# Performance work log

Hardware: AMD Instinct MI355X
Metric: run time of the kernel (lower is better)

## Reference

```python
import jax, jax.numpy as jnp
import numpy as np

TOP_K = 2

def setup_inputs() -> dict:
    key = jax.random.key(0)
    ks = jax.random.split(key, 8)
    B, S, H, E, F = 4, 2048, 1024, 8, 2048  # F = hidden * expansion(2)
    scale_in = 0.02
    return {
        "x": jax.random.normal(ks[0], (B, S, H), dtype=jnp.float32),
        "router_w": jax.random.normal(ks[1], (H, E), dtype=jnp.float32) * scale_in,
        "router_b": jnp.zeros((E,), dtype=jnp.float32),
        "w1": jax.random.normal(ks[2], (E, H, F), dtype=jnp.float32) * scale_in,
        "b1": jnp.zeros((E, F), dtype=jnp.float32),
        "w2": jax.random.normal(ks[3], (E, F, H), dtype=jnp.float32) * scale_in,
        "b2": jnp.zeros((E, H), dtype=jnp.float32),
    }

def reference(x, router_w, router_b, w1, b1, w2, b2):
    B, S, H = x.shape
    E = router_b.shape[0]
    T = B * S
    flat = x.reshape(T, H)
    # Router + top-k gating (softmax over the k selected logits, as in torch code)
    logits = flat @ router_w + router_b                       # [T, E]
    topk_scores, topk_idx = jax.lax.top_k(logits, TOP_K)      # [T, k]
    probs = jax.nn.softmax(topk_scores, axis=-1)              # [T, k]
    # Dense gate matrix: gates[t, e] = prob if e selected for token t else 0
    gates = jnp.zeros((T, E), dtype=flat.dtype).at[
        jnp.arange(T)[:, None], topk_idx
    ].add(probs)                                              # [T, E]
    # Expert FFNs computed as batched GEMMs over the expert axis
    h = jax.nn.relu(jnp.einsum('td,edf->etf', flat, w1) + b1[:, None, :])  # [E, T, F]
    eout = jnp.einsum('etf,efd->etd', h, w2) + b2[:, None, :]              # [E, T, H]
    out = jnp.einsum('etd,te->td', eout, gates)                            # [T, H]
    return out.reshape(B, S, H)
```

## Files before the change

### kernel.cpp

```cpp
#include <hip/hip_runtime.h>
#include <hip/hip_bf16.h>

#define T_TOK 8192
#define HDIM 1024
#define FDIM 2048
#define NEXP 8
#define NASSIGN (T_TOK * 2)
#define ROWCAP (NASSIGN + 256)
#define NHB 64
#define MAXT 136
#define MAXT2 72

typedef __bf16 bf16;
typedef __bf16 bf16x4 __attribute__((ext_vector_type(4)));
typedef __bf16 bf16x8 __attribute__((ext_vector_type(8)));
typedef float f32x4 __attribute__((ext_vector_type(4)));

__device__ __forceinline__ void gload_lds16(const void* g, void* l) {
    __builtin_amdgcn_global_load_lds(
        (const __attribute__((address_space(1))) void*)(uintptr_t)g,
        (__attribute__((address_space(3))) void*)(uintptr_t)l,
        16, 0, 0);
}

__global__ __launch_bounds__(256) void transpose_to_bf16(
    const float* __restrict__ in, bf16* __restrict__ out, int R, int C) {
    __shared__ float tile[64][68];
    int e = blockIdx.z;
    const float* inp = in + (size_t)e * R * C;
    bf16* outp = out + (size_t)e * R * C;
    int c0 = blockIdx.x * 64, r0 = blockIdx.y * 64;
    int tid = threadIdx.x;
    int tx = tid & 15, ty = tid >> 4;
#pragma unroll
    for (int i = 0; i < 4; i++) {
        int row = ty + i * 16;
        float4 v = *(const float4*)&inp[(size_t)(r0 + row) * C + c0 + tx * 4];
        *(float4*)&tile[row][tx * 4] = v;
    }
    __syncthreads();
#pragma unroll
    for (int i = 0; i < 2; i++) {
        int idx = tid + i * 256;
        int c = idx >> 3, seg = idx & 7;
        bf16x8 v;
#pragma unroll
        for (int j = 0; j < 8; j++) v[j] = (bf16)tile[seg * 8 + j][c];
        *(bf16x8*)&outp[(size_t)(c0 + c) * R + r0 + seg * 8] = v;
    }
}

__global__ __launch_bounds__(256) void router_kernel(
    const float* __restrict__ x, const float* __restrict__ rw,
    const float* __restrict__ rb, int* __restrict__ expert_pair,
    float2* __restrict__ gate_pair) {
    __shared__ float rwT[NEXP][HDIM];
    __shared__ float rbs[NEXP];
    int tid = threadIdx.x;
    for (int i = tid; i < HDIM * NEXP / 4; i += 256) {
        float4 v = ((const float4*)rw)[i];
        int h = i >> 1, e0 = (i & 1) * 4;
        rwT[e0 + 0][h] = v.x;
        rwT[e0 + 1][h] = v.y;
        rwT[e0 + 2][h] = v.z;
        rwT[e0 + 3][h] = v.w;
    }
    if (tid < NEXP) rbs[tid] = rb[tid];
    __syncthreads();
    int wave = tid >> 6, lane = tid & 63;
    int tbase = blockIdx.x * 32 + wave * 8;

    for (int tk = 0; tk < 8; tk++) {
        int t = tbase + tk;
        const float4* xt = (const float4*)(x + (size_t)t * HDIM);
        float p[NEXP];
#pragma unroll
        for (int e = 0; e < NEXP; e++) p[e] = 0.f;
#pragma unroll
        for (int it = 0; it < 4; it++) {
            float4 v = xt[it * 64 + lane];
            int h = (it * 64 + lane) * 4;
#pragma unroll
            for (int e = 0; e < NEXP; e++) {
                float4 wv = *(const float4*)&rwT[e][h];
                p[e] += v.x * wv.x + v.y * wv.y + v.z * wv.z + v.w * wv.w;
            }
        }
#pragma unroll
        for (int off = 32; off >= 1; off >>= 1) {
#pragma unroll
            for (int e = 0; e < NEXP; e++) p[e] += __shfl_xor(p[e], off, 64);
        }
        if (lane == 0) {
            float lg[NEXP];
#pragma unroll
            for (int e = 0; e < NEXP; e++) lg[e] = p[e] + rbs[e];
            int e0 = 0;
#pragma unroll
            for (int e = 1; e < NEXP; e++)
                if (lg[e] > lg[e0]) e0 = e;
            int e1 = -1;
#pragma unroll
            for (int e = 0; e < NEXP; e++) {
                if (e == e0) continue;
                if (e1 < 0 || lg[e] > lg[e1]) e1 = e;
            }
            float z = expf(lg[e1] - lg[e0]);
            expert_pair[t] = e0 | (e1 << 16);
            gate_pair[t] = make_float2(1.f / (1.f + z), z / (1.f + z));
        }
    }
}

__global__ __launch_bounds__(256) void hist_kernel(
    const int* __restrict__ expert_pair, int* __restrict__ hist) {
    int tid = threadIdx.x;
    int wave = tid >> 6, lane = tid & 63;
    int a = blockIdx.x * 256 + tid;
    int t = a >> 1, j = a & 1;
    int e = (expert_pair[t] >> (16 * j)) & 0xffff;
    __shared__ int wcnt[4][NEXP];
#pragma unroll
    for (int ee = 0; ee < NEXP; ee++) {
        unsigned long long m = __ballot(e == ee);
        if (lane == 0) wcnt[wave][ee] = __popcll(m);
    }
    __syncthreads();
    if (tid < NEXP)
        hist[blockIdx.x * NEXP + tid] =
            wcnt[0][tid] + wcnt[1][tid] + wcnt[2][tid] + wcnt[3][tid];
}

__global__ __launch_bounds__(256) void scan_kernel(
    const int* __restrict__ hist, int* __restrict__ start,
    int* __restrict__ cnt, int* __restrict__ offs,
    int* __restrict__ tile_e2, int* __restrict__ tile_m2,
    int* __restrict__ ntiles2) {
    __shared__ int h[NHB * NEXP];
    __shared__ int tot[NEXP];
    __shared__ int offsh[NEXP];
    int tid = threadIdx.x;
    for (int i = tid; i < NHB * NEXP; i += 256) h[i] = hist[i];
    __syncthreads();
    if (tid < NEXP) {
        int s = 0;
        for (int b = 0; b < NHB; b++) s += h[b * NEXP + tid];
        tot[tid] = s;
        cnt[tid] = s;
    }
    __syncthreads();
    if (tid == 0) {
        int o = 0;
        for (int e = 0; e < NEXP; e++) {
            offsh[e] = o;
            offs[e] = o;
            o += tot[e];
        }
        int idx2 = 0;
        for (int e = 0; e < NEXP; e++) {
            int nt = (tot[e] + 255) >> 8;
            for (int m = 0; m < nt; m++) {
                tile_e2[idx2] = e;
                tile_m2[idx2] = m;
                idx2++;
            }
        }
        ntiles2[0] = idx2;
    }
    __syncthreads();
    if (tid < NEXP) {
        int run = offsh[tid];
        for (int b = 0; b < NHB; b++) {
            start[b * NEXP + tid] = run;
            run += h[b * NEXP + tid];
        }
    }
}

__global__ __launch_bounds__(256) void scatter_kernel(
    const int* __restrict__ expert_pair, const float2* __restrict__ gate_pair,
    const int* __restrict__ start, int* __restrict__ perm,
    float* __restrict__ gatebuf, int* __restrict__ rowbuf) {
    int tid = threadIdx.x;
    int wave = tid >> 6, lane = tid & 63;
    int a = blockIdx.x * 256 + tid;
    int t = a >> 1, j = a & 1;
    int e = (expert_pair[t] >> (16 * j)) & 0xffff;
    float2 gp = gate_pair[t];
    float g = j ? gp.y : gp.x;
    __shared__ int wcnt[4][NEXP];
    int rankw = 0;
    unsigned long long below = (1ull << lane) - 1ull;
#pragma unroll
    for (int ee = 0; ee < NEXP; ee++) {
        unsigned long long m = __ballot(e == ee);
        if (lane == 0) wcnt[wave][ee] = __popcll(m);
        if (ee == e) rankw = __popcll(m & below);
    }
    __syncthreads();
    int cross = 0;
    for (int w = 0; w < wave; w++) cross += wcnt[w][e];
    int pos = start[blockIdx.x * NEXP + e] + cross + rankw;
    perm[pos] = t;
    gatebuf[pos] = g;
    rowbuf[a] = pos;
}

__global__ __launch_bounds__(256) void pack_kernel(
    const float* __restrict__ x, const int* __restrict__ perm,
    bf16* __restrict__ xg) {
    int r0 = blockIdx.x * 16;
    int wave = threadIdx.x >> 6, lane = threadIdx.x & 63;
#pragma unroll
    for (int i = 0; i < 4; i++) {
        int row = r0 + wave * 4 + i;
        int tok = perm[row];
        const float* src = x + (size_t)tok * HDIM;
        bf16* dst = xg + (size_t)row * HDIM;
#pragma unroll
        for (int it = 0; it < 4; it++) {
            int c = (it * 64 + lane) * 4;
            float4 v = *(const float4*)&src[c];
            bf16x4 b = {(bf16)v.x, (bf16)v.y, (bf16)v.z, (bf16)v.w};
            *(bf16x4*)&dst[c] = b;
        }
    }
}

template <bool RELU, bool GATE, int K, int N>
__global__ __launch_bounds__(512, 4) void moe_gemm_p(
    const bf16* __restrict__ A, const bf16* __restrict__ B,
    const float* __restrict__ bias, const float* __restrict__ gates,
    bf16* __restrict__ out, const int* __restrict__ cnt,
    const int* __restrict__ offs, const int* __restrict__ tile_e2,
    const int* __restrict__ tile_m2, const int* __restrict__ ntiles2) {
    constexpr int NT = N / 128;
    constexpr int nk = K / 32;
    int ntl = ntiles2[0];
    int nact = ntl * NT;
    int f = blockIdx.x;
    if (f >= nact) return;
    int q8 = nact >> 3, r8 = nact & 7;
    int xcd = f & 7, rest = f >> 3;
    int wg = (xcd < r8) ? (xcd * (q8 + 1) + rest)
                        : (r8 * (q8 + 1) + (xcd - r8) * q8 + rest);
    int tile = wg / NT, ncol = wg - tile * NT;
    int e = tile_e2[tile];
    int n_cnt = cnt[e];
    int off_e = offs[e];
    int m0 = tile_m2[tile] * 256;
    int n0 = ncol * 128;

    __shared__ bf16 As[3][256][32];
    __shared__ bf16 Bs[3][128][32];

    int tid = threadIdx.x;
    int lane = tid & 63;
    int wave = tid >> 6;
    int wm = wave & 1;
    int wn = wave >> 1;
    int quad = lane >> 4, l16 = lane & 15;
    int rsw = (quad ^ ((l16 >> 1) & 3)) * 8;

    const bf16* Ae = A + (size_t)off_e * K;
    const bf16* Be = B + (size_t)e * (size_t)N * K;

    int r0s = tid >> 2;
    int segs = (tid & 3) ^ ((tid >> 3) & 3);
    const bf16* agA0 = Ae + (size_t)(m0 + r0s) * K + segs * 8;
    const bf16* agA1 = Ae + (size_t)(m0 + 128 + r0s) * K + segs * 8;
    const bf16* bgB0 = Be + (size_t)(n0 + r0s) * K + segs * 8;

    auto STG = [&](int buf, int kt) {
        bf16* Ab = (bf16*)As + (size_t)buf * (256 * 32);
        bf16* Bb = (bf16*)Bs + (size_t)buf * (128 * 32);
        gload_lds16(agA0 + (size_t)kt * 32, Ab + (wave * 64) * 8);
        gload_lds16(agA1 + (size_t)kt * 32, Ab + (512 + wave * 64) * 8);
        gload_lds16(bgB0 + (size_t)kt * 32, Bb + (wave * 64) * 8);
    };

    f32x4 acc[8][2];
#pragma unroll
    for (int i = 0; i < 8; i++)
#pragma unroll
        for (int j = 0; j < 2; j++) acc[i][j] = f32x4{0.f, 0.f, 0.f, 0.f};

    STG(0, 0);
    STG(1, 1);

    int b = 0, bs = 2;
    for (int t = 0; t < nk; t++) {
        if (t + 2 < nk) {
            STG(bs, t + 2);
            asm volatile("s_waitcnt vmcnt(6)" ::: "memory");
        } else if (t + 2 == nk) {
            asm volatile("s_waitcnt vmcnt(3)" ::: "memory");
        } else {
            asm volatile("s_waitcnt vmcnt(0)" ::: "memory");
        }
        asm volatile("s_barrier" ::: "memory");

        const bf16* Ab = (const bf16*)As + (size_t)b * (256 * 32);
        const bf16* Bb = (const bf16*)Bs + (size_t)b * (128 * 32);
        bf16x8 bf0 = *(const bf16x8*)(Bb + (wn * 32 + 0 * 16 + l16) * 32 + rsw);
        bf16x8 bf1 = *(const bf16x8*)(Bb + (wn * 32 + 1 * 16 + l16) * 32 + rsw);
        bf16x8 af[4];
#pragma unroll
        for (int mi = 0; mi < 4; mi++)
            af[mi] = *(const bf16x8*)(Ab + (wm * 128 + mi * 16 + l16) * 32 + rsw);
        asm volatile("s_waitcnt lgkmcnt(0)" ::: "memory");
        __builtin_amdgcn_s_setprio(1);
#pragma unroll
        for (int mi = 0; mi < 4; mi++) {
            acc[mi][0] = __builtin_amdgcn_mfma_f32_16x16x32_bf16(af[mi], bf0, acc[mi][0], 0, 0, 0);
            acc[mi][1] = __builtin_amdgcn_mfma_f32_16x16x32_bf16(af[mi], bf1, acc[mi][1], 0, 0, 0);
        }
        __builtin_amdgcn_s_setprio(0);
#pragma unroll
        for (int mi = 0; mi < 4; mi++)
            af[mi] = *(const bf16x8*)(Ab + (wm * 128 + (4 + mi) * 16 + l16) * 32 + rsw);
        asm volatile("s_waitcnt lgkmcnt(0)" ::: "memory");
        __builtin_amdgcn_s_setprio(1);
#pragma unroll
        for (int mi = 0; mi < 4; mi++) {
            acc[4 + mi][0] = __builtin_amdgcn_mfma_f32_16x16x32_bf16(af[mi], bf0, acc[4 + mi][0], 0, 0, 0);
            acc[4 + mi][1] = __builtin_amdgcn_mfma_f32_16x16x32_bf16(af[mi], bf1, acc[4 + mi][1], 0, 0, 0);
        }
        __builtin_amdgcn_s_setprio(0);
        asm volatile("s_barrier" ::: "memory");

        b = (b == 2) ? 0 : b + 1;
        bs = (bs == 2) ? 0 : bs + 1;
    }

#pragma unroll
    for (int mi = 0; mi < 8; mi++)
#pragma unroll
        for (int nj = 0; nj < 2; nj++)
#pragma unroll
            for (int r = 0; r < 4; r++) {
                int m = m0 + wm * 128 + mi * 16 + quad * 4 + r;
                if (m < n_cnt) {
                    int n = n0 + wn * 32 + nj * 16 + l16;
                    float v = acc[mi][nj][r] + bias[e * N + n];
                    if (RELU) v = v > 0.f ? v : 0.f;
                    if (GATE) v *= gates[off_e + m];
                    out[(size_t)(off_e + m) * N + n] = (bf16)v;
                }
            }
}

__global__ __launch_bounds__(256) void combine_kernel(
    const bf16* __restrict__ eout, const int* __restrict__ rowbuf,
    float* __restrict__ out) {
    int t = blockIdx.x;
    int r0 = rowbuf[2 * t], r1 = rowbuf[2 * t + 1];
    const bf16* p0 = eout + (size_t)r0 * HDIM;
    const bf16* p1 = eout + (size_t)r1 * HDIM;
    float* o = out + (size_t)t * HDIM;
    int n = threadIdx.x * 4;
    bf16x4 a = *(const bf16x4*)&p0[n];
    bf16x4 b = *(const bf16x4*)&p1[n];
    float4 v = {(float)a[0] + (float)b[0], (float)a[1] + (float)b[1],
                (float)a[2] + (float)b[2], (float)a[3] + (float)b[3]};
    *(float4*)&o[n] = v;
}

extern "C" void kernel_launch(void* const* d_in, const int* in_sizes, int n_in,
                              void* d_out, int out_size, void* d_ws, size_t ws_size,
                              hipStream_t stream) {
    const float* x = (const float*)d_in[0];
    const float* rw = (const float*)d_in[1];
    const float* rb = (const float*)d_in[2];
    const float* w1 = (const float*)d_in[3];
    const float* b1 = (const float*)d_in[4];
    const float* w2 = (const float*)d_in[5];
    const float* b2 = (const float*)d_in[6];
    float* out = (float*)d_out;

    char* ws = (char*)d_ws;
    size_t o = 0;
    auto alloc = [&](size_t bytes) {
        char* p = ws + o;
        o += (bytes + 255) & ~(size_t)255;
        return p;
    };
    bf16* w1t = (bf16*)alloc((size_t)NEXP * FDIM * HDIM * 2);
    bf16* w2t = (bf16*)alloc((size_t)NEXP * HDIM * FDIM * 2);
    bf16* hbuf = (bf16*)alloc((size_t)ROWCAP * FDIM * 2);
    bf16* xg = (bf16*)alloc((size_t)ROWCAP * HDIM * 2);
    bf16* eout = xg;
    int* expert_pair = (int*)alloc((size_t)T_TOK * 4);
    float2* gate_pair = (float2*)alloc((size_t)T_TOK * 8);
    int* hist = (int*)alloc((size_t)NHB * NEXP * 4);
    int* start = (int*)alloc((size_t)NHB * NEXP * 4);
    int* perm = (int*)alloc((size_t)NASSIGN * 4);
    float* gatebuf = (float*)alloc((size_t)NASSIGN * 4);
    int* rowbuf = (int*)alloc((size_t)NASSIGN * 4);
    int* cnt = (int*)alloc(256);
    int* offs = (int*)alloc(256);
    int* tile_e2 = (int*)alloc((size_t)MAXT2 * 4);
    int* tile_m2 = (int*)alloc((size_t)MAXT2 * 4);
    int* ntiles2 = (int*)alloc(256);

    transpose_to_bf16<<<dim3(FDIM / 64, HDIM / 64, NEXP), 256, 0, stream>>>(w1, w1t, HDIM, FDIM);
    transpose_to_bf16<<<dim3(HDIM / 64, FDIM / 64, NEXP), 256, 0, stream>>>(w2, w2t, FDIM, HDIM);
    router_kernel<<<T_TOK / 32, 256, 0, stream>>>(x, rw, rb, expert_pair, gate_pair);
    hist_kernel<<<NHB, 256, 0, stream>>>(expert_pair, hist);
    scan_kernel<<<1, 256, 0, stream>>>(hist, start, cnt, offs, tile_e2, tile_m2, ntiles2);
    scatter_kernel<<<NHB, 256, 0, stream>>>(expert_pair, gate_pair, start, perm, gatebuf, rowbuf);
    pack_kernel<<<NASSIGN / 16, 256, 0, stream>>>(x, perm, xg);
    moe_gemm_p<true, false, HDIM, FDIM><<<dim3(MAXT2 * (FDIM / 128)), 512, 0, stream>>>(
        xg, w1t, b1, nullptr, hbuf, cnt, offs, tile_e2, tile_m2, ntiles2);
    moe_gemm_p<false, true, FDIM, HDIM><<<dim3(MAXT2 * (HDIM / 128)), 512, 0, stream>>>(
        hbuf, w2t, b2, gatebuf, eout, cnt, offs, tile_e2, tile_m2, ntiles2);
    combine_kernel<<<T_TOK, 256, 0, stream>>>(eout, rowbuf, out);
}
```

Measured before the change: 458.8 us.

## Use 4-wave GEMM blocks with 128x64 per-wave tiles for more register reuse

```diff
diff --git a/kernel.cpp b/kernel.cpp
--- a/kernel.cpp
+++ b/kernel.cpp
@@ -8,7 +8,6 @@
 #define NASSIGN (T_TOK * 2)
 #define ROWCAP (NASSIGN + 256)
 #define NHB 64
-#define MAXT 136
 #define MAXT2 72
 
 typedef __bf16 bf16;
@@ -228,7 +227,7 @@
 }
 
 template <bool RELU, bool GATE, int K, int N>
-__global__ __launch_bounds__(512, 4) void moe_gemm_p(
+__global__ __launch_bounds__(256, 2) void moe_gemm_p(
     const bf16* __restrict__ A, const bf16* __restrict__ B,
     const float* __restrict__ bias, const float* __restrict__ gates,
     bf16* __restrict__ out, const int* __restrict__ cnt,
@@ -267,23 +266,27 @@
 
     int r0s = tid >> 2;
     int segs = (tid & 3) ^ ((tid >> 3) & 3);
-    const bf16* agA0 = Ae + (size_t)(m0 + r0s) * K + segs * 8;
-    const bf16* agA1 = Ae + (size_t)(m0 + 128 + r0s) * K + segs * 8;
-    const bf16* bgB0 = Be + (size_t)(n0 + r0s) * K + segs * 8;
+    const bf16* agA = Ae + (size_t)(m0 + r0s) * K + segs * 8;
+    const bf16* bgB = Be + (size_t)(n0 + r0s) * K + segs * 8;
 
     auto STG = [&](int buf, int kt) {
         bf16* Ab = (bf16*)As + (size_t)buf * (256 * 32);
         bf16* Bb = (bf16*)Bs + (size_t)buf * (128 * 32);
-        gload_lds16(agA0 + (size_t)kt * 32, Ab + (wave * 64) * 8);
-        gload_lds16(agA1 + (size_t)kt * 32, Ab + (512 + wave * 64) * 8);
-        gload_lds16(bgB0 + (size_t)kt * 32, Bb + (wave * 64) * 8);
+#pragma unroll
+        for (int j = 0; j < 4; j++)
+            gload_lds16(agA + (size_t)(j * 64) * K + (size_t)kt * 32,
+                        Ab + wave * 512 + j * 2048);
+#pragma unroll
+        for (int j = 0; j < 2; j++)
+            gload_lds16(bgB + (size_t)(j * 64) * K + (size_t)kt * 32,
+                        Bb + wave * 512 + j * 2048);
     };
 
-    f32x4 acc[8][2];
+    f32x4 acc[8][4];
 #pragma unroll
     for (int i = 0; i < 8; i++)
 #pragma unroll
-        for (int j = 0; j < 2; j++) acc[i][j] = f32x4{0.f, 0.f, 0.f, 0.f};
+        for (int j = 0; j < 4; j++) acc[i][j] = f32x4{0.f, 0.f, 0.f, 0.f};
 
     STG(0, 0);
     STG(1, 1);
@@ -292,9 +295,9 @@
     for (int t = 0; t < nk; t++) {
         if (t + 2 < nk) {
             STG(bs, t + 2);
+            asm volatile("s_waitcnt vmcnt(12)" ::: "memory");
+        } else if (t + 2 == nk) {
             asm volatile("s_waitcnt vmcnt(6)" ::: "memory");
-        } else if (t + 2 == nk) {
-            asm volatile("s_waitcnt vmcnt(3)" ::: "memory");
         } else {
             asm volatile("s_waitcnt vmcnt(0)" ::: "memory");
         }
@@ -302,30 +305,21 @@
 
         const bf16* Ab = (const bf16*)As + (size_t)b * (256 * 32);
         const bf16* Bb = (const bf16*)Bs + (size_t)b * (128 * 32);
-        bf16x8 bf0 = *(const bf16x8*)(Bb + (wn * 32 + 0 * 16 + l16) * 32 + rsw);
-        bf16x8 bf1 = *(const bf16x8*)(Bb + (wn * 32 + 1 * 16 + l16) * 32 + rsw);
-        bf16x8 af[4];
-#pragma unroll
-        for (int mi = 0; mi < 4; mi++)
+        bf16x8 bfv[4];
+#pragma unroll
+        for (int nj = 0; nj < 4; nj++)
+            bfv[nj] = *(const bf16x8*)(Bb + (wn * 64 + nj * 16 + l16) * 32 + rsw);
+        bf16x8 af[8];
+#pragma unroll
+        for (int mi = 0; mi < 8; mi++)
             af[mi] = *(const bf16x8*)(Ab + (wm * 128 + mi * 16 + l16) * 32 + rsw);
-        asm volatile("s_waitcnt lgkmcnt(0)" ::: "memory");
         __builtin_amdgcn_s_setprio(1);
 #pragma unroll
-        for (int mi = 0; mi < 4; mi++) {
-            acc[mi][0] = __builtin_amdgcn_mfma_f32_16x16x32_bf16(af[mi], bf0, acc[mi][0], 0, 0, 0);
-            acc[mi][1] = __builtin_amdgcn_mfma_f32_16x16x32_bf16(af[mi], bf1, acc[mi][1], 0, 0, 0);
-        }
-        __builtin_amdgcn_s_setprio(0);
-#pragma unroll
-        for (int mi = 0; mi < 4; mi++)
-            af[mi] = *(const bf16x8*)(Ab + (wm * 128 + (4 + mi) * 16 + l16) * 32 + rsw);
-        asm volatile("s_waitcnt lgkmcnt(0)" ::: "memory");
-        __builtin_amdgcn_s_setprio(1);
-#pragma unroll
-        for (int mi = 0; mi < 4; mi++) {
-            acc[4 + mi][0] = __builtin_amdgcn_mfma_f32_16x16x32_bf16(af[mi], bf0, acc[4 + mi][0], 0, 0, 0);
-            acc[4 + mi][1] = __builtin_amdgcn_mfma_f32_16x16x32_bf16(af[mi], bf1, acc[4 + mi][1], 0, 0, 0);
-        }
+        for (int mi = 0; mi < 8; mi++)
+#pragma unroll
+            for (int nj = 0; nj < 4; nj++)
+                acc[mi][nj] = __builtin_amdgcn_mfma_f32_16x16x32_bf16(
+                    af[mi], bfv[nj], acc[mi][nj], 0, 0, 0);
         __builtin_amdgcn_s_setprio(0);
         asm volatile("s_barrier" ::: "memory");
 
@@ -336,12 +330,12 @@
 #pragma unroll
     for (int mi = 0; mi < 8; mi++)
 #pragma unroll
-        for (int nj = 0; nj < 2; nj++)
+        for (int nj = 0; nj < 4; nj++)
 #pragma unroll
             for (int r = 0; r < 4; r++) {
                 int m = m0 + wm * 128 + mi * 16 + quad * 4 + r;
                 if (m < n_cnt) {
-                    int n = n0 + wn * 32 + nj * 16 + l16;
+                    int n = n0 + wn * 64 + nj * 16 + l16;
                     float v = acc[mi][nj][r] + bias[e * N + n];
                     if (RELU) v = v > 0.f ? v : 0.f;
                     if (GATE) v *= gates[off_e + m];
@@ -410,9 +404,9 @@
     scan_kernel<<<1, 256, 0, stream>>>(hist, start, cnt, offs, tile_e2, tile_m2, ntiles2);
     scatter_kernel<<<NHB, 256, 0, stream>>>(expert_pair, gate_pair, start, perm, gatebuf, rowbuf);
     pack_kernel<<<NASSIGN / 16, 256, 0, stream>>>(x, perm, xg);
-    moe_gemm_p<true, false, HDIM, FDIM><<<dim3(MAXT2 * (FDIM / 128)), 512, 0, stream>>>(
+    moe_gemm_p<true, false, HDIM, FDIM><<<dim3(MAXT2 * (FDIM / 128)), 256, 0, stream>>>(
         xg, w1t, b1, nullptr, hbuf, cnt, offs, tile_e2, tile_m2, ntiles2);
-    moe_gemm_p<false, true, FDIM, HDIM><<<dim3(MAXT2 * (HDIM / 128)), 512, 0, stream>>>(
+    moe_gemm_p<false, true, FDIM, HDIM><<<dim3(MAXT2 * (HDIM / 128)), 256, 0, stream>>>(
         hbuf, w2t, b2, gatebuf, eout, cnt, offs, tile_e2, tile_m2, ntiles2);
     combine_kernel<<<T_TOK, 256, 0, stream>>>(eout, rowbuf, out);
 }
```

After: 493.9 us. +7.7%, slower.

## Fuse histogram and bf16 cast into router, gather rows inside first GEMM

Applied to the files above, without the earlier changes.

```diff
diff --git a/kernel.cpp b/kernel.cpp
--- a/kernel.cpp
+++ b/kernel.cpp
@@ -7,8 +7,7 @@
 #define NEXP 8
 #define NASSIGN (T_TOK * 2)
 #define ROWCAP (NASSIGN + 256)
-#define NHB 64
-#define MAXT 136
+#define NHB 256
 #define MAXT2 72
 
 typedef __bf16 bf16;
@@ -53,9 +52,11 @@
 __global__ __launch_bounds__(256) void router_kernel(
     const float* __restrict__ x, const float* __restrict__ rw,
     const float* __restrict__ rb, int* __restrict__ expert_pair,
-    float2* __restrict__ gate_pair) {
+    float2* __restrict__ gate_pair, bf16* __restrict__ xb,
+    int* __restrict__ hist) {
     __shared__ float rwT[NEXP][HDIM];
     __shared__ float rbs[NEXP];
+    __shared__ int sh_pair[32];
     int tid = threadIdx.x;
     for (int i = tid; i < HDIM * NEXP / 4; i += 256) {
         float4 v = ((const float4*)rw)[i];
@@ -79,6 +80,8 @@
 #pragma unroll
         for (int it = 0; it < 4; it++) {
             float4 v = xt[it * 64 + lane];
+            bf16x4 bv = {(bf16)v.x, (bf16)v.y, (bf16)v.z, (bf16)v.w};
+            *(bf16x4*)&xb[(size_t)t * HDIM + (it * 64 + lane) * 4] = bv;
             int h = (it * 64 + lane) * 4;
 #pragma unroll
             for (int e = 0; e < NEXP; e++) {
@@ -106,29 +109,22 @@
                 if (e1 < 0 || lg[e] > lg[e1]) e1 = e;
             }
             float z = expf(lg[e1] - lg[e0]);
-            expert_pair[t] = e0 | (e1 << 16);
+            int pair = e0 | (e1 << 16);
+            expert_pair[t] = pair;
+            sh_pair[wave * 8 + tk] = pair;
             gate_pair[t] = make_float2(1.f / (1.f + z), z / (1.f + z));
         }
     }
-}
-
-__global__ __launch_bounds__(256) void hist_kernel(
-    const int* __restrict__ expert_pair, int* __restrict__ hist) {
-    int tid = threadIdx.x;
-    int wave = tid >> 6, lane = tid & 63;
-    int a = blockIdx.x * 256 + tid;
-    int t = a >> 1, j = a & 1;
-    int e = (expert_pair[t] >> (16 * j)) & 0xffff;
-    __shared__ int wcnt[4][NEXP];
-#pragma unroll
-    for (int ee = 0; ee < NEXP; ee++) {
-        unsigned long long m = __ballot(e == ee);
-        if (lane == 0) wcnt[wave][ee] = __popcll(m);
-    }
-    __syncthreads();
-    if (tid < NEXP)
-        hist[blockIdx.x * NEXP + tid] =
-            wcnt[0][tid] + wcnt[1][tid] + wcnt[2][tid] + wcnt[3][tid];
+    __syncthreads();
+    if (wave == 0) {
+        int tl = lane >> 1, j = lane & 1;
+        int e = (sh_pair[tl] >> (16 * j)) & 0xffff;
+#pragma unroll
+        for (int ee = 0; ee < NEXP; ee++) {
+            unsigned long long m = __ballot(e == ee);
+            if (lane == ee) hist[blockIdx.x * NEXP + ee] = __popcll(m);
+        }
+    }
 }
 
 __global__ __launch_bounds__(256) void scan_kernel(
@@ -177,63 +173,37 @@
     }
 }
 
-__global__ __launch_bounds__(256) void scatter_kernel(
+__global__ __launch_bounds__(64) void scatter_kernel(
     const int* __restrict__ expert_pair, const float2* __restrict__ gate_pair,
     const int* __restrict__ start, int* __restrict__ perm,
     float* __restrict__ gatebuf, int* __restrict__ rowbuf) {
-    int tid = threadIdx.x;
-    int wave = tid >> 6, lane = tid & 63;
-    int a = blockIdx.x * 256 + tid;
+    int lane = threadIdx.x;
+    int a = blockIdx.x * 64 + lane;
     int t = a >> 1, j = a & 1;
     int e = (expert_pair[t] >> (16 * j)) & 0xffff;
     float2 gp = gate_pair[t];
     float g = j ? gp.y : gp.x;
-    __shared__ int wcnt[4][NEXP];
-    int rankw = 0;
+    int rank = 0;
     unsigned long long below = (1ull << lane) - 1ull;
 #pragma unroll
     for (int ee = 0; ee < NEXP; ee++) {
         unsigned long long m = __ballot(e == ee);
-        if (lane == 0) wcnt[wave][ee] = __popcll(m);
-        if (ee == e) rankw = __popcll(m & below);
-    }
-    __syncthreads();
-    int cross = 0;
-    for (int w = 0; w < wave; w++) cross += wcnt[w][e];
-    int pos = start[blockIdx.x * NEXP + e] + cross + rankw;
+        if (ee == e) rank = __popcll(m & below);
+    }
+    int pos = start[blockIdx.x * NEXP + e] + rank;
     perm[pos] = t;
     gatebuf[pos] = g;
     rowbuf[a] = pos;
 }
 
-__global__ __launch_bounds__(256) void pack_kernel(
-    const float* __restrict__ x, const int* __restrict__ perm,
-    bf16* __restrict__ xg) {
-    int r0 = blockIdx.x * 16;
-    int wave = threadIdx.x >> 6, lane = threadIdx.x & 63;
-#pragma unroll
-    for (int i = 0; i < 4; i++) {
-        int row = r0 + wave * 4 + i;
-        int tok = perm[row];
-        const float* src = x + (size_t)tok * HDIM;
-        bf16* dst = xg + (size_t)row * HDIM;
-#pragma unroll
-        for (int it = 0; it < 4; it++) {
-            int c = (it * 64 + lane) * 4;
-            float4 v = *(const float4*)&src[c];
-            bf16x4 b = {(bf16)v.x, (bf16)v.y, (bf16)v.z, (bf16)v.w};
-            *(bf16x4*)&dst[c] = b;
-        }
-    }
-}
-
-template <bool RELU, bool GATE, int K, int N>
+template <bool RELU, bool GATE, bool GATHER, int K, int N>
 __global__ __launch_bounds__(512, 4) void moe_gemm_p(
     const bf16* __restrict__ A, const bf16* __restrict__ B,
     const float* __restrict__ bias, const float* __restrict__ gates,
     bf16* __restrict__ out, const int* __restrict__ cnt,
     const int* __restrict__ offs, const int* __restrict__ tile_e2,
-    const int* __restrict__ tile_m2, const int* __restrict__ ntiles2) {
+    const int* __restrict__ tile_m2, const int* __restrict__ ntiles2,
+    const int* __restrict__ perm) {
     constexpr int NT = N / 128;
     constexpr int nk = K / 32;
     int ntl = ntiles2[0];
@@ -262,13 +232,24 @@
     int quad = lane >> 4, l16 = lane & 15;
     int rsw = (quad ^ ((l16 >> 1) & 3)) * 8;
 
-    const bf16* Ae = A + (size_t)off_e * K;
     const bf16* Be = B + (size_t)e * (size_t)N * K;
 
     int r0s = tid >> 2;
     int segs = (tid & 3) ^ ((tid >> 3) & 3);
-    const bf16* agA0 = Ae + (size_t)(m0 + r0s) * K + segs * 8;
-    const bf16* agA1 = Ae + (size_t)(m0 + 128 + r0s) * K + segs * 8;
+    const bf16* agA0;
+    const bf16* agA1;
+    if (GATHER) {
+        int g0 = off_e + m0 + r0s;
+        int g1 = off_e + m0 + 128 + r0s;
+        g0 = g0 < NASSIGN ? g0 : NASSIGN - 1;
+        g1 = g1 < NASSIGN ? g1 : NASSIGN - 1;
+        agA0 = A + (size_t)perm[g0] * K + segs * 8;
+        agA1 = A + (size_t)perm[g1] * K + segs * 8;
+    } else {
+        const bf16* Ae = A + (size_t)off_e * K;
+        agA0 = Ae + (size_t)(m0 + r0s) * K + segs * 8;
+        agA1 = Ae + (size_t)(m0 + 128 + r0s) * K + segs * 8;
+    }
     const bf16* bgB0 = Be + (size_t)(n0 + r0s) * K + segs * 8;
 
     auto STG = [&](int buf, int kt) {
@@ -353,17 +334,21 @@
 __global__ __launch_bounds__(256) void combine_kernel(
     const bf16* __restrict__ eout, const int* __restrict__ rowbuf,
     float* __restrict__ out) {
-    int t = blockIdx.x;
+    int c = blockIdx.x * 256 + threadIdx.x;
+    int t = c >> 7;
+    int n = (c & 127) * 8;
     int r0 = rowbuf[2 * t], r1 = rowbuf[2 * t + 1];
-    const bf16* p0 = eout + (size_t)r0 * HDIM;
-    const bf16* p1 = eout + (size_t)r1 * HDIM;
-    float* o = out + (size_t)t * HDIM;
-    int n = threadIdx.x * 4;
-    bf16x4 a = *(const bf16x4*)&p0[n];
-    bf16x4 b = *(const bf16x4*)&p1[n];
-    float4 v = {(float)a[0] + (float)b[0], (float)a[1] + (float)b[1],
-                (float)a[2] + (float)b[2], (float)a[3] + (float)b[3]};
-    *(float4*)&o[n] = v;
+    const bf16* p0 = eout + (size_t)r0 * HDIM + n;
+    const bf16* p1 = eout + (size_t)r1 * HDIM + n;
+    bf16x8 a = *(const bf16x8*)p0;
+    bf16x8 b = *(const bf16x8*)p1;
+    float* o = out + (size_t)t * HDIM + n;
+    float4 v0 = {(float)a[0] + (float)b[0], (float)a[1] + (float)b[1],
+                 (float)a[2] + (float)b[2], (float)a[3] + (float)b[3]};
+    float4 v1 = {(float)a[4] + (float)b[4], (float)a[5] + (float)b[5],
+                 (float)a[6] + (float)b[6], (float)a[7] + (float)b[7]};
+    *(float4*)o = v0;
+    *(float4*)(o + 4) = v1;
 }
 
 extern "C" void kernel_launch(void* const* d_in, const int* in_sizes, int n_in,
@@ -388,8 +373,8 @@
     bf16* w1t = (bf16*)alloc((size_t)NEXP * FDIM * HDIM * 2);
     bf16* w2t = (bf16*)alloc((size_t)NEXP * HDIM * FDIM * 2);
     bf16* hbuf = (bf16*)alloc((size_t)ROWCAP * FDIM * 2);
-    bf16* xg = (bf16*)alloc((size_t)ROWCAP * HDIM * 2);
-    bf16* eout = xg;
+    bf16* eout = (bf16*)alloc((size_t)ROWCAP * HDIM * 2);
+    bf16* xb = (bf16*)alloc((size_t)T_TOK * HDIM * 2);
     int* expert_pair = (int*)alloc((size_t)T_TOK * 4);
     float2* gate_pair = (float2*)alloc((size_t)T_TOK * 8);
     int* hist = (int*)alloc((size_t)NHB * NEXP * 4);
@@ -405,14 +390,12 @@
 
     transpose_to_bf16<<<dim3(FDIM / 64, HDIM / 64, NEXP), 256, 0, stream>>>(w1, w1t, HDIM, FDIM);
     transpose_to_bf16<<<dim3(HDIM / 64, FDIM / 64, NEXP), 256, 0, stream>>>(w2, w2t, FDIM, HDIM);
-    router_kernel<<<T_TOK / 32, 256, 0, stream>>>(x, rw, rb, expert_pair, gate_pair);
-    hist_kernel<<<NHB, 256, 0, stream>>>(expert_pair, hist);
+    router_kernel<<<NHB, 256, 0, stream>>>(x, rw, rb, expert_pair, gate_pair, xb, hist);
     scan_kernel<<<1, 256, 0, stream>>>(hist, start, cnt, offs, tile_e2, tile_m2, ntiles2);
-    scatter_kernel<<<NHB, 256, 0, stream>>>(expert_pair, gate_pair, start, perm, gatebuf, rowbuf);
-    pack_kernel<<<NASSIGN / 16, 256, 0, stream>>>(x, perm, xg);
-    moe_gemm_p<true, false, HDIM, FDIM><<<dim3(MAXT2 * (FDIM / 128)), 512, 0, stream>>>(
-        xg, w1t, b1, nullptr, hbuf, cnt, offs, tile_e2, tile_m2, ntiles2);
-    moe_gemm_p<false, true, FDIM, HDIM><<<dim3(MAXT2 * (HDIM / 128)), 512, 0, stream>>>(
-        hbuf, w2t, b2, gatebuf, eout, cnt, offs, tile_e2, tile_m2, ntiles2);
-    combine_kernel<<<T_TOK, 256, 0, stream>>>(eout, rowbuf, out);
-}
+    scatter_kernel<<<NHB, 64, 0, stream>>>(expert_pair, gate_pair, start, perm, gatebuf, rowbuf);
+    moe_gemm_p<true, false, true, HDIM, FDIM><<<dim3(MAXT2 * (FDIM / 128)), 512, 0, stream>>>(
+        xb, w1t, b1, nullptr, hbuf, cnt, offs, tile_e2, tile_m2, ntiles2, perm);
+    moe_gemm_p<false, true, false, FDIM, HDIM><<<dim3(MAXT2 * (HDIM / 128)), 512, 0, stream>>>(
+        hbuf, w2t, b2, gatebuf, eout, cnt, offs, tile_e2, tile_m2, ntiles2, nullptr);
+    combine_kernel<<<T_TOK * HDIM / 8 / 256, 256, 0, stream>>>(eout, rowbuf, out);
+}
```

After: 449.1 us. 2.1% less time.
